# Performance work log

Hardware: AMD Instinct MI355X
Metric: run time of the kernel (lower is better)

## Reference

```python
import jax, jax.numpy as jnp
import numpy as np

# ---- static config (mirrors LSSTransform defaults) ----
B, N, CIN, CT = 4, 6, 512, 64
OGH, OGW, DS = 256, 704, 16
FH, FW = OGH // DS, OGW // DS            # 16, 44
DB0, DB1, DBS = 4.0, 45.0, 1.0
D = int((DB1 - DB0) / DBS)               # 41 depth bins
NXX, NYY, NZZ = 128, 128, 1              # BEV grid from x/y/z bounds
DXv = np.array([0.8, 0.8, 20.0], np.float32)            # dx
BXv = np.array([-51.2 + 0.4, -51.2 + 0.4, 0.0], np.float32)  # bx = lower + dx/2


def _frustum():
    # (D, fH, fW, 3) of (pixel_u, pixel_v, depth), as in create_frustum
    ds = np.broadcast_to(np.arange(DB0, DB1, DBS, dtype=np.float32)[:, None, None], (D, FH, FW))
    xs = np.broadcast_to(np.linspace(0, OGW - 1, FW, dtype=np.float32)[None, None, :], (D, FH, FW))
    ys = np.broadcast_to(np.linspace(0, OGH - 1, FH, dtype=np.float32)[None, :, None], (D, FH, FW))
    return jnp.asarray(np.stack([xs, ys, ds], axis=-1))

FRUSTUM = _frustum()


def setup_inputs() -> dict:
    key = jax.random.key(0)
    k0, k1, k2 = jax.random.split(key, 3)
    x = jax.random.normal(k0, (B, N, CIN, FH, FW), jnp.float32)
    # camera->ego rotation: ego = (z_cam, x_cam, y_cam), so depth maps to ego-x
    R = jnp.array([[0., 0., 1.], [1., 0., 0.], [0., 1., 0.]], jnp.float32)
    rots = jnp.broadcast_to(R, (B, N, 3, 3)) + 0.0
    trans = 0.5 * jax.random.normal(k1, (B, N, 3), jnp.float32)
    K = jnp.array([[500., 0., OGW / 2.], [0., 500., OGH / 2.], [0., 0., 1.]], jnp.float32)
    intrins = jnp.broadcast_to(K, (B, N, 3, 3)) + 0.0
    post_rots = jnp.broadcast_to(jnp.eye(3, dtype=jnp.float32), (B, N, 3, 3)) + 0.0
    post_trans = jnp.zeros((B, N, 3), jnp.float32)
    Wd = 0.02 * jax.random.normal(k2, (D + CT, CIN), jnp.float32)  # depthnet 1x1 conv weight
    bd = jnp.zeros((D + CT,), jnp.float32)
    return dict(x=x, rots=rots, trans=trans, intrins=intrins,
                post_rots=post_rots, post_trans=post_trans, Wd=Wd, bd=bd)


def _forward(x, rots, trans, intrins, post_rots, post_trans, Wd, bd):
    # depthnet: 1x1 conv == channel matmul
    feat = jnp.einsum('bnchw,oc->bnohw', x, Wd) + bd[None, None, :, None, None]
    depth = jax.nn.softmax(feat[:, :, :D], axis=2)          # (B,N,D,H,W)
    cvt = feat[:, :, D:D + CT]                              # (B,N,CT,H,W)
    vol = depth[:, :, None] * cvt[:, :, :, None]            # (B,N,CT,D,H,W)
    vol = jnp.transpose(vol, (0, 1, 3, 4, 5, 2))            # (B,N,D,H,W,CT)

    # get_geometry: undo image augs, unproject, cam->ego
    pts = FRUSTUM[None, None] - post_trans[:, :, None, None, None, :]
    pts = jnp.einsum('bnij,bndhwj->bndhwi', jnp.linalg.inv(post_rots), pts)
    pts = jnp.concatenate([pts[..., :2] * pts[..., 2:3], pts[..., 2:3]], axis=-1)
    comb = rots @ jnp.linalg.inv(intrins)
    pts = jnp.einsum('bnij,bndhwj->bndhwi', comb, pts) + trans[:, :, None, None, None, :]

    # voxel_pooling: truncating cast matches torch .long()
    g = ((pts - (jnp.asarray(BXv) - jnp.asarray(DXv) / 2.0)) / jnp.asarray(DXv)).astype(jnp.int32)
    gx, gy, gz = g[..., 0], g[..., 1], g[..., 2]
    kept = (gx >= 0) & (gx < NXX) & (gy >= 0) & (gy < NYY) & (gz >= 0) & (gz < NZZ)
    bix = jnp.arange(B, dtype=jnp.int32)[:, None, None, None, None]
    vox = ((bix * NZZ + gz) * NYY + gy) * NXX + gx          # flat voxel id per point
    TOT = B * NZZ * NYY * NXX
    seg = jnp.where(kept, vox, TOT).reshape(-1)             # invalid -> trash bucket
    feats = vol.reshape(-1, CT)                             # (Nprime, CT)
    sums = jax.ops.segment_sum(feats, seg, num_segments=TOT + 1)[:TOT]
    final = sums.reshape(B, NZZ, NYY, NXX, CT)
    # (B, C, nz, ny, nx) then cat over z into channels -> (B, nz*C, ny, nx)
    final = jnp.transpose(final, (0, 1, 4, 2, 3)).reshape(B, NZZ * CT, NYY, NXX)
    return final


def reference(x, rots, trans, intrins, post_rots, post_trans, Wd, bd):
    return _forward(x, rots, trans, intrins, post_rots, post_trans, Wd, bd)
```

## Files before the change

kernel.cpp:

```cpp
#include <hip/hip_runtime.h>
#include <hip/hip_bf16.h>
#include <math.h>

#define B_   4
#define N_   6
#define CIN  512
#define CT   64
#define Dd   41
#define FH   16
#define FW   44
#define NPIX 704
#define NO   105
#define DSTR 48
#define NXX  128
#define NYY  128
#define NZZ  1
#define TOT  (B_*NZZ*NYY*NXX)
#define NK   (TOT*8)
#define NPTS (B_*N_*Dd*NPIX)
#define NCHUNK ((NPTS+63)/64)

#define WSTRIDE 520

typedef __attribute__((ext_vector_type(8))) short short8;
typedef __attribute__((ext_vector_type(4))) float f32x4;


__device__ __forceinline__ unsigned short f2bf(float f) {
    unsigned u = __float_as_uint(f);
    u += 0x7FFFu + ((u >> 16) & 1u);
    return (unsigned short)(u >> 16);
}

__device__ __forceinline__ void inv3(const double* m, double* o) {
    double a=m[0],b=m[1],c=m[2],d=m[3],e=m[4],f=m[5],g=m[6],h=m[7],i=m[8];
    double A  =  (e*i - f*h);
    double Bc = -(d*i - f*g);
    double Cc =  (d*h - e*g);
    double det = a*A + b*Bc + c*Cc;
    double inv = 1.0/det;
    o[0]=A*inv;            o[1]=-(b*i - c*h)*inv;  o[2]= (b*f - c*e)*inv;
    o[3]=Bc*inv;           o[4]= (a*i - c*g)*inv;  o[5]=-(a*f - c*d)*inv;
    o[6]=Cc*inv;           o[7]=-(a*h - b*g)*inv;  o[8]= (a*e - b*d)*inv;
}

__device__ __forceinline__ void geom_lane(const double* s_tf, int b, int pix, int l,
                                          bool& kept, int& vox) {
    const int hh = pix / FW, ww = pix % FW;
    const double fx = (double)((float)(ww * (703.0/43.0)));
    const double fy = (double)((float)(hh * 17.0));
    const double px = fx - s_tf[21], py = fy - s_tf[22], mz = -s_tf[23];
    const double qx0 = s_tf[ 9]*px + s_tf[10]*py + s_tf[11]*mz, qx1 = s_tf[11];
    const double qy0 = s_tf[12]*px + s_tf[13]*py + s_tf[14]*mz, qy1 = s_tf[14];
    const double qz0 = s_tf[15]*px + s_tf[16]*py + s_tf[17]*mz, qz1 = s_tf[17];
    const double ux0 = s_tf[0]*qx0 + s_tf[1]*qy0 + s_tf[2], ux1 = s_tf[0]*qx1 + s_tf[1]*qy1;
    const double uy0 = s_tf[3]*qx0 + s_tf[4]*qy0 + s_tf[5], uy1 = s_tf[3]*qx1 + s_tf[4]*qy1;
    const double uz0 = s_tf[6]*qx0 + s_tf[7]*qy0 + s_tf[8], uz1 = s_tf[6]*qx1 + s_tf[7]*qy1;
    const double t0 = s_tf[18], t1 = s_tf[19], t2 = s_tf[20];

    const double DXD = (double)0.8f;
    const double LOX = (double)(-50.8f) - DXD*0.5;
    const double LOY = LOX;
    const double DZD = 20.0;
    const double LOZ = -10.0;

    kept = false; vox = 0;
    if (l < Dd) {
        double fz = 4.0 + (double)l;
        double qz = qz0 + qz1*fz;
        double sx = qz*(ux0 + ux1*fz) + t0;
        double sy = qz*(uy0 + uy1*fz) + t1;
        double sz = qz*(uz0 + uz1*fz) + t2;
        int gx = (int)((sx - LOX) / DXD);
        int gy = (int)((sy - LOY) / DXD);
        int gz = (int)((sz - LOZ) / DZD);
        kept = (gx>=0) & (gx<NXX) & (gy>=0) & (gy<NYY) & (gz>=0) & (gz<NZZ);
        vox  = (((b*NZZ + gz)*NYY + gy)*NXX + gx);
    }
}

__global__ __launch_bounds__(256) void prep_kernel(
    const float* __restrict__ rots, const float* __restrict__ trans,
    const float* __restrict__ intrins, const float* __restrict__ post_rots,
    const float* __restrict__ post_trans, const float* __restrict__ Wd,
    const float* __restrict__ x,
    double* __restrict__ tf, unsigned short* __restrict__ WdB,
    unsigned short* __restrict__ xB)
{
    const int t = threadIdx.x;
    if (blockIdx.x < 2112) {
        __shared__ float s_x[64*65];
        const int p    = blockIdx.x;
        const int bn   = p / 88;
        const int r    = p % 88;
        const int kg   = r / 11;
        const int tile = r % 11;
        const int pix0 = tile * 64;

        const float* src = x + ((size_t)bn*CIN + kg*64)*NPIX + pix0;
        #pragma unroll
        for (int i = 0; i < 16; i++) {
            int idx = i*256 + t;
            int k  = idx >> 6;
            int px = idx & 63;
            s_x[k*65 + px] = src[(size_t)k*NPIX + px];
        }
        __syncthreads();

        const int px  = t & 63;
        #pragma unroll
        for (int pass = 0; pass < 2; pass++) {
            int k8l = (t >> 6) + 4*pass;
            unsigned pk[4];
            #pragma unroll
            for (int i = 0; i < 4; i++) {
                float a = s_x[(k8l*8 + 2*i    )*65 + px];
                float c = s_x[(k8l*8 + 2*i + 1)*65 + px];
                pk[i] = (unsigned)f2bf(a) | ((unsigned)f2bf(c) << 16);
            }
            unsigned* dst = (unsigned*)&xB[(((size_t)(bn*64 + kg*8 + k8l))*NPIX + pix0 + px)*8];
            *(uint4*)dst = make_uint4(pk[0], pk[1], pk[2], pk[3]);
        }
    } else {
        int b2 = blockIdx.x - 2112;
        int idx = b2*256 + t;
        if (idx < 128*CIN) {
            int o = idx / CIN;
            WdB[idx] = (o < NO) ? f2bf(Wd[idx]) : (unsigned short)0;
        }
        if (b2 == 0 && t < B_*N_) {
            int bn = t;
            double k[9], pr[9], r[9], ik[9], ipr[9], c[9];
            for (int i=0;i<9;i++) { k[i]=intrins[bn*9+i]; pr[i]=post_rots[bn*9+i]; r[i]=rots[bn*9+i]; }
            inv3(k, ik);
            inv3(pr, ipr);
            for (int i=0;i<3;i++)
                for (int j=0;j<3;j++) {
                    double s = 0.0;
                    for (int kk=0;kk<3;kk++) s += r[i*3+kk]*ik[kk*3+j];
                    c[i*3+j] = s;
                }
            double* o = tf + bn*24;
            for (int i=0;i<9;i++) o[i]   = c[i];
            for (int i=0;i<9;i++) o[9+i] = ipr[i];
            for (int i=0;i<3;i++) o[18+i] = (double)trans[bn*3+i];
            for (int i=0;i<3;i++) o[21+i] = (double)post_trans[bn*3+i];
        }
    }
}

__global__ __launch_bounds__(256) void gemm_kernel(
    const unsigned short* __restrict__ xB, const unsigned short* __restrict__ WdB,
    const float* __restrict__ bd,
    float* __restrict__ featD, float* __restrict__ featB)
{
    __shared__ unsigned short s_wd[32*WSTRIDE];

    const int t    = threadIdx.x;
    const int l    = t & 63;
    const int wv   = t >> 6;
    const int col  = l & 15;
    const int quad = l >> 4;

    const int xcd = blockIdx.x & 7;
    const int q   = blockIdx.x >> 3;
    const int s   = q & 3;
    const int pg  = q >> 2;
    const int p   = pg*8 + xcd;
    const int bn   = p / 11;
    const int tile = p % 11;
    const int pix0 = tile * 64;

    {
        const int o  = t >> 3;
        const int c8 = t & 7;
        const unsigned short* srcw = WdB + (size_t)(s*32 + o)*CIN;
        #pragma unroll
        for (int i = 0; i < 8; i++) {
            int k = c8*8 + i*64;
            *(uint4*)&s_wd[o*WSTRIDE + k] = *(const uint4*)&srcw[k];
        }
    }
    __syncthreads();

    f32x4 acc[2];
    acc[0] = (f32x4){0.f,0.f,0.f,0.f};
    acc[1] = (f32x4){0.f,0.f,0.f,0.f};

    const int pix = pix0 + wv*16 + col;
    const unsigned short* xbase = xB + (((size_t)(bn*64) )*NPIX)*8;

    #pragma unroll
    for (int ks = 0; ks < 16; ks++) {
        const int k8 = ks*4 + quad;
        short8 bfr = *(const short8*)&xbase[((size_t)k8*NPIX + pix)*8];
        #pragma unroll
        for (int j = 0; j < 2; j++) {
            short8 afr = *(const short8*)&s_wd[(j*16 + col)*WSTRIDE + ks*32 + quad*8];
            acc[j] = __builtin_amdgcn_mfma_f32_16x16x32_bf16(afr, bfr, acc[j], 0, 0, 0);
        }
    }

    const size_t prow = (size_t)(bn*NPIX + pix);
    #pragma unroll
    for (int j = 0; j < 2; j++) {
        #pragma unroll
        for (int rr = 0; rr < 4; rr++) {
            int o = (2*s + j)*16 + quad*4 + rr;
            if (o < Dd) {
                featD[prow*DSTR + o] = acc[j][rr] + bd[o];
            } else if (o < NO) {
                featB[prow*CT + (o - Dd)] = acc[j][rr] + bd[o];
            }
        }
    }
}

__global__ __launch_bounds__(256) void geom_hist_kernel(
    const double* __restrict__ tf, int* __restrict__ hist8,
    int* __restrict__ rank_arr)
{
    __shared__ double s_tf[24];
    const int bid = (blockIdx.x & 7) * 528 + (blockIdx.x >> 3);
    const int t   = threadIdx.x;
    const int l   = t & 63;
    const int wv  = t >> 6;
    const int bn  = bid / 176;
    const int pix = (bid % 176)*4 + wv;
    const int b   = bn / N_;

    if (t < 24) s_tf[t] = tf[bn*24 + t];
    __syncthreads();

    bool kept; int vox;
    geom_lane(s_tf, b, pix, l, kept, vox);
    if (kept) {
        int key = vox*8 + (pix & 7);
        int rank = atomicAdd(&hist8[key], 1);
        rank_arr[(size_t)(bn*NPIX + pix)*Dd + l] = rank;
    }
}

__global__ __launch_bounds__(256) void scan1_kernel(const int* __restrict__ hist8,
                                                    int* __restrict__ offs8,
                                                    int* __restrict__ bsum) {
    __shared__ int s[256];
    const int t = threadIdx.x;
    const int i = blockIdx.x*256 + t;
    int val = hist8[i];
    s[t] = val;
    __syncthreads();
    #pragma unroll
    for (int off = 1; off < 256; off <<= 1) {
        int u = (t >= off) ? s[t-off] : 0;
        __syncthreads();
        s[t] += u;
        __syncthreads();
    }
    offs8[i] = s[t] - val;
    if (t == 255) bsum[blockIdx.x] = s[255];
}

__global__ __launch_bounds__(1024) void scan2_kernel(int* __restrict__ bsum,
                                                     int* __restrict__ np) {
    __shared__ int s[1024];
    const int t = threadIdx.x;
    int a = bsum[2*t], b = bsum[2*t+1];
    s[t] = a + b;
    __syncthreads();
    #pragma unroll
    for (int off = 1; off < 1024; off <<= 1) {
        int u = (t >= off) ? s[t-off] : 0;
        __syncthreads();
        s[t] += u;
        __syncthreads();
    }
    int excl = s[t] - (a + b);
    bsum[2*t]   = excl;
    bsum[2*t+1] = excl + a;
    if (t == 1023) np[0] = s[1023];
}

__global__ __launch_bounds__(256) void sm_scatter_kernel(
    const float* __restrict__ featD, const double* __restrict__ tf,
    const int* __restrict__ offs8, const int* __restrict__ bsum,
    const int* __restrict__ rank_arr, uint2* __restrict__ rec)
{
    __shared__ double s_tf[24];
    const int bid = (blockIdx.x & 7) * 528 + (blockIdx.x >> 3);
    const int t   = threadIdx.x;
    const int l   = t & 63;
    const int wv  = t >> 6;
    const int bn  = bid / 176;
    const int pix = (bid % 176)*4 + wv;
    const int b   = bn / N_;

    if (t < 24) s_tf[t] = tf[bn*24 + t];
    __syncthreads();

    const size_t prow = (size_t)(bn*NPIX + pix);

    float logit = (l < Dd) ? featD[prow*DSTR + l] : -3.0e38f;
    float mm = logit;
    #pragma unroll
    for (int off = 32; off > 0; off >>= 1) mm = fmaxf(mm, __shfl_xor(mm, off));
    float e = (l < Dd) ? expf(logit - mm) : 0.0f;
    float ssum = e;
    #pragma unroll
    for (int off = 32; off > 0; off >>= 1) ssum += __shfl_xor(ssum, off);
    const float wgt = e / ssum;

    bool kept; int vox;
    geom_lane(s_tf, b, pix, l, kept, vox);
    if (kept) {
        int key = vox*8 + (pix & 7);
        int pos = offs8[key] + bsum[key >> 8] + rank_arr[prow*Dd + l];
        unsigned pk = ((unsigned)vox << 15) | (unsigned)prow;
        rec[pos] = make_uint2(pk, __float_as_uint(wgt));
    }
}

__global__ __launch_bounds__(256) void gather_kernel(
    const uint2* __restrict__ rec, const int* __restrict__ np,
    const float* __restrict__ featB, float* __restrict__ scat)
{
    const int bid = (blockIdx.x & 7) * 339 + (blockIdx.x >> 3);
    const int t  = threadIdx.x;
    const int wv = t >> 6;
    const int l  = t & 63;
    const int chunk = bid * 4 + wv;
    const int base  = chunk * 64;
    const int Np = np[0];
    if (base >= Np) return;
    int cnt = Np - base; if (cnt > 64) cnt = 64;

    unsigned pk = 0; float w = 0.0f;
    if (l < cnt) { uint2 r = rec[base + l]; pk = r.x; w = __uint_as_float(r.y); }
    unsigned pkm = __shfl(pk, (l == 0) ? 0 : (l - 1));
    unsigned long long starts =
        __ballot((l > 0) && (l < cnt) && ((pk >> 15) != (pkm >> 15)));

    unsigned long long m = starts;
    int rs = 0;
    while (rs < cnt) {
        int re = m ? (__ffsll((unsigned long long)m) - 1) : cnt;
        if (m) m &= m - 1;
        float acc = 0.0f;
        for (int j = rs; j < re; j++) {
            unsigned pkj = __shfl(pk, j);
            float    wj  = __shfl(w, j);
            unsigned id  = pkj & 0x7FFFu;
            acc += wj * featB[(size_t)id * CT + l];
        }
        unsigned vrun = __shfl(pk, rs) >> 15;
        float* dst = scat + (size_t)vrun * CT + l;
        if (rs == 0 || re == cnt) {
            unsafeAtomicAdd(dst, acc);
        } else {
            *dst = acc;
        }
        rs = re;
    }
}

__global__ __launch_bounds__(256) void transpose_k(const float* __restrict__ scat,
                                                   float* __restrict__ out) {
    __shared__ float tile[64][65];
    int b  = blockIdx.x >> 8;
    int t0 = (blockIdx.x & 255) * 64;
    const float* src = scat + (size_t)b * (NYY*NXX) * CT;
    #pragma unroll
    for (int i=0;i<16;i++) {
        int idx = threadIdx.x + i*256;
        int p = idx >> 6, c = idx & 63;
        tile[p][c] = src[(size_t)(t0+p)*CT + c];
    }
    __syncthreads();
    float* dst = out + (size_t)b * CT * (NYY*NXX);
    #pragma unroll
    for (int i=0;i<16;i++) {
        int idx = threadIdx.x + i*256;
        int c = idx >> 6, p = idx & 63;
        dst[(size_t)c*(NYY*NXX) + t0 + p] = tile[p][c];
    }
}

extern "C" void kernel_launch(void* const* d_in, const int* in_sizes, int n_in,
                              void* d_out, int out_size, void* d_ws, size_t ws_size,
                              hipStream_t stream) {
    const float* x          = (const float*)d_in[0];
    const float* rots       = (const float*)d_in[1];
    const float* trans      = (const float*)d_in[2];
    const float* intrins    = (const float*)d_in[3];
    const float* post_rots  = (const float*)d_in[4];
    const float* post_trans = (const float*)d_in[5];
    const float* Wd         = (const float*)d_in[6];
    const float* bd         = (const float*)d_in[7];
    float* out = (float*)d_out;

    char* ws = (char*)d_ws;
    float*          featB  = (float*)ws;          ws += (size_t)B_*N_*NPIX*CT*4;
    float*          featD  = (float*)ws;          ws += (size_t)B_*N_*NPIX*DSTR*4;
    char*           Xreg   = ws;                  ws += (size_t)B_*N_*CIN*NPIX*2;
    int*            rank_a = (int*)ws;            ws += (size_t)NPTS*4;
    uint2*          rec    = (uint2*)ws;          ws += (size_t)NPTS*8;
    int*            hist8  = (int*)ws;            ws += (size_t)NK*4;
    int*            offs8  = (int*)ws;            ws += (size_t)NK*4;
    int*            bsum   = (int*)ws;            ws += 2048*4;
    int*            np     = (int*)ws;            ws += 256;
    double*         tf     = (double*)ws;         ws += (size_t)B_*N_*24*8;
    unsigned short* WdB    = (unsigned short*)ws; ws += (size_t)128*CIN*2;

    unsigned short* xB   = (unsigned short*)Xreg;
    float*          scat = (float*)Xreg;

    hipMemsetAsync(hist8, 0, (size_t)NK*4, stream);
    prep_kernel<<<2368, 256, 0, stream>>>(rots, trans, intrins, post_rots, post_trans,
                                          Wd, x, tf, WdB, xB);
    gemm_kernel<<<1056, 256, 0, stream>>>(xB, WdB, bd, featD, featB);
    geom_hist_kernel<<<B_*N_*176, 256, 0, stream>>>(tf, hist8, rank_a);
    hipMemsetAsync(scat, 0, (size_t)TOT*CT*4, stream);
    scan1_kernel<<<NK/256, 256, 0, stream>>>(hist8, offs8, bsum);
    scan2_kernel<<<1, 1024, 0, stream>>>(bsum, np);
    sm_scatter_kernel<<<B_*N_*176, 256, 0, stream>>>(featD, tf, offs8, bsum, rank_a, rec);
    gather_kernel<<<2712, 256, 0, stream>>>(rec, np, featB, scat);
    transpose_k<<<B_*(NYY*NXX/64), 256, 0, stream>>>(scat, out);
}
```

Baseline: 220.9 us.

## Fuse GEMM and geometry histogram launches, drop 8-way sub-bucketed histogram

Merges the depthnet GEMM and the geometry/histogram kernel into one launch whose blocks branch on their index, so the two independent stages can overlap on the GPU. The histogram is also reduced from eight sub-buckets per voxel (keyed by pixel) to one counter per voxel. This shrinks the memset, both scan passes and the offset lookups. In exchange, more atomics land on the same address, and the order in which records within a voxel are sorted changes.

```diff
diff --git a/kernel.cpp b/kernel.cpp
--- a/kernel.cpp
+++ b/kernel.cpp
@@ -16,11 +16,13 @@
 #define NYY  128
 #define NZZ  1
 #define TOT  (B_*NZZ*NYY*NXX)
-#define NK   (TOT*8)
 #define NPTS (B_*N_*Dd*NPIX)
 #define NCHUNK ((NPTS+63)/64)
 
 #define WSTRIDE 520
+
+#define GEMM_BLOCKS 1056
+#define GEOM_BLOCKS 4224
 
 typedef __attribute__((ext_vector_type(8))) short short8;
 typedef __attribute__((ext_vector_type(4))) float f32x4;
@@ -149,105 +151,100 @@
     }
 }
 
-__global__ __launch_bounds__(256) void gemm_kernel(
+__global__ __launch_bounds__(256) void gemm_geom_kernel(
     const unsigned short* __restrict__ xB, const unsigned short* __restrict__ WdB,
-    const float* __restrict__ bd,
-    float* __restrict__ featD, float* __restrict__ featB)
+    const float* __restrict__ bd, const double* __restrict__ tf,
+    float* __restrict__ featD, float* __restrict__ featB,
+    int* __restrict__ hist, int* __restrict__ rank_arr)
 {
     __shared__ unsigned short s_wd[32*WSTRIDE];
+    __shared__ double s_tf[24];
 
     const int t    = threadIdx.x;
     const int l    = t & 63;
     const int wv   = t >> 6;
-    const int col  = l & 15;
-    const int quad = l >> 4;
-
-    const int xcd = blockIdx.x & 7;
-    const int q   = blockIdx.x >> 3;
-    const int s   = q & 3;
-    const int pg  = q >> 2;
-    const int p   = pg*8 + xcd;
-    const int bn   = p / 11;
-    const int tile = p % 11;
-    const int pix0 = tile * 64;
-
-    {
-        const int o  = t >> 3;
-        const int c8 = t & 7;
-        const unsigned short* srcw = WdB + (size_t)(s*32 + o)*CIN;
+
+    if (blockIdx.x < GEMM_BLOCKS) {
+        const int col  = l & 15;
+        const int quad = l >> 4;
+        const int xcd = blockIdx.x & 7;
+        const int q   = blockIdx.x >> 3;
+        const int s   = q & 3;
+        const int pg  = q >> 2;
+        const int p   = pg*8 + xcd;
+        const int bn   = p / 11;
+        const int tile = p % 11;
+        const int pix0 = tile * 64;
+
+        {
+            const int o  = t >> 3;
+            const int c8 = t & 7;
+            const unsigned short* srcw = WdB + (size_t)(s*32 + o)*CIN;
+            #pragma unroll
+            for (int i = 0; i < 8; i++) {
+                int k = c8*8 + i*64;
+                *(uint4*)&s_wd[o*WSTRIDE + k] = *(const uint4*)&srcw[k];
+            }
+        }
+        __syncthreads();
+
+        f32x4 acc[2];
+        acc[0] = (f32x4){0.f,0.f,0.f,0.f};
+        acc[1] = (f32x4){0.f,0.f,0.f,0.f};
+
+        const int pix = pix0 + wv*16 + col;
+        const unsigned short* xbase = xB + (((size_t)(bn*64))*NPIX)*8;
+
         #pragma unroll
-        for (int i = 0; i < 8; i++) {
-            int k = c8*8 + i*64;
-            *(uint4*)&s_wd[o*WSTRIDE + k] = *(const uint4*)&srcw[k];
-        }
-    }
-    __syncthreads();
-
-    f32x4 acc[2];
-    acc[0] = (f32x4){0.f,0.f,0.f,0.f};
-    acc[1] = (f32x4){0.f,0.f,0.f,0.f};
-
-    const int pix = pix0 + wv*16 + col;
-    const unsigned short* xbase = xB + (((size_t)(bn*64) )*NPIX)*8;
-
-    #pragma unroll
-    for (int ks = 0; ks < 16; ks++) {
-        const int k8 = ks*4 + quad;
-        short8 bfr = *(const short8*)&xbase[((size_t)k8*NPIX + pix)*8];
+        for (int ks = 0; ks < 16; ks++) {
+            const int k8 = ks*4 + quad;
+            short8 bfr = *(const short8*)&xbase[((size_t)k8*NPIX + pix)*8];
+            #pragma unroll
+            for (int j = 0; j < 2; j++) {
+                short8 afr = *(const short8*)&s_wd[(j*16 + col)*WSTRIDE + ks*32 + quad*8];
+                acc[j] = __builtin_amdgcn_mfma_f32_16x16x32_bf16(afr, bfr, acc[j], 0, 0, 0);
+            }
+        }
+
+        const size_t prow = (size_t)(bn*NPIX + pix);
         #pragma unroll
         for (int j = 0; j < 2; j++) {
-            short8 afr = *(const short8*)&s_wd[(j*16 + col)*WSTRIDE + ks*32 + quad*8];
-            acc[j] = __builtin_amdgcn_mfma_f32_16x16x32_bf16(afr, bfr, acc[j], 0, 0, 0);
-        }
-    }
-
-    const size_t prow = (size_t)(bn*NPIX + pix);
-    #pragma unroll
-    for (int j = 0; j < 2; j++) {
-        #pragma unroll
-        for (int rr = 0; rr < 4; rr++) {
-            int o = (2*s + j)*16 + quad*4 + rr;
-            if (o < Dd) {
-                featD[prow*DSTR + o] = acc[j][rr] + bd[o];
-            } else if (o < NO) {
-                featB[prow*CT + (o - Dd)] = acc[j][rr] + bd[o];
+            #pragma unroll
+            for (int rr = 0; rr < 4; rr++) {
+                int o = (2*s + j)*16 + quad*4 + rr;
+                if (o < Dd) {
+                    featD[prow*DSTR + o] = acc[j][rr] + bd[o];
+                } else if (o < NO) {
+                    featB[prow*CT + (o - Dd)] = acc[j][rr] + bd[o];
+                }
             }
         }
-    }
-}
-
-__global__ __launch_bounds__(256) void geom_hist_kernel(
-    const double* __restrict__ tf, int* __restrict__ hist8,
-    int* __restrict__ rank_arr)
-{
-    __shared__ double s_tf[24];
-    const int bid = (blockIdx.x & 7) * 528 + (blockIdx.x >> 3);
-    const int t   = threadIdx.x;
-    const int l   = t & 63;
-    const int wv  = t >> 6;
-    const int bn  = bid / 176;
-    const int pix = (bid % 176)*4 + wv;
-    const int b   = bn / N_;
-
-    if (t < 24) s_tf[t] = tf[bn*24 + t];
-    __syncthreads();
-
-    bool kept; int vox;
-    geom_lane(s_tf, b, pix, l, kept, vox);
-    if (kept) {
-        int key = vox*8 + (pix & 7);
-        int rank = atomicAdd(&hist8[key], 1);
-        rank_arr[(size_t)(bn*NPIX + pix)*Dd + l] = rank;
-    }
-}
-
-__global__ __launch_bounds__(256) void scan1_kernel(const int* __restrict__ hist8,
-                                                    int* __restrict__ offs8,
+    } else {
+        const int bid2 = blockIdx.x - GEMM_BLOCKS;
+        const int bid  = (bid2 & 7) * 528 + (bid2 >> 3);
+        const int bn  = bid / 176;
+        const int pix = (bid % 176)*4 + wv;
+        const int b   = bn / N_;
+
+        if (t < 24) s_tf[t] = tf[bn*24 + t];
+        __syncthreads();
+
+        bool kept; int vox;
+        geom_lane(s_tf, b, pix, l, kept, vox);
+        if (kept) {
+            int rank = atomicAdd(&hist[vox], 1);
+            rank_arr[(size_t)(bn*NPIX + pix)*Dd + l] = rank;
+        }
+    }
+}
+
+__global__ __launch_bounds__(256) void scan1_kernel(const int* __restrict__ hist,
+                                                    int* __restrict__ offs,
                                                     int* __restrict__ bsum) {
     __shared__ int s[256];
     const int t = threadIdx.x;
     const int i = blockIdx.x*256 + t;
-    int val = hist8[i];
+    int val = hist[i];
     s[t] = val;
     __syncthreads();
     #pragma unroll
@@ -257,33 +254,31 @@
         s[t] += u;
         __syncthreads();
     }
-    offs8[i] = s[t] - val;
+    offs[i] = s[t] - val;
     if (t == 255) bsum[blockIdx.x] = s[255];
 }
 
-__global__ __launch_bounds__(1024) void scan2_kernel(int* __restrict__ bsum,
-                                                     int* __restrict__ np) {
-    __shared__ int s[1024];
+__global__ __launch_bounds__(256) void scan2_kernel(int* __restrict__ bsum,
+                                                    int* __restrict__ np) {
+    __shared__ int s[256];
     const int t = threadIdx.x;
-    int a = bsum[2*t], b = bsum[2*t+1];
-    s[t] = a + b;
+    int v = bsum[t];
+    s[t] = v;
     __syncthreads();
     #pragma unroll
-    for (int off = 1; off < 1024; off <<= 1) {
+    for (int off = 1; off < 256; off <<= 1) {
         int u = (t >= off) ? s[t-off] : 0;
         __syncthreads();
         s[t] += u;
         __syncthreads();
     }
-    int excl = s[t] - (a + b);
-    bsum[2*t]   = excl;
-    bsum[2*t+1] = excl + a;
-    if (t == 1023) np[0] = s[1023];
+    bsum[t] = s[t] - v;
+    if (t == 255) np[0] = s[255];
 }
 
 __global__ __launch_bounds__(256) void sm_scatter_kernel(
     const float* __restrict__ featD, const double* __restrict__ tf,
-    const int* __restrict__ offs8, const int* __restrict__ bsum,
+    const int* __restrict__ offs, const int* __restrict__ bsum,
     const int* __restrict__ rank_arr, uint2* __restrict__ rec)
 {
     __shared__ double s_tf[24];
@@ -313,8 +308,7 @@
     bool kept; int vox;
     geom_lane(s_tf, b, pix, l, kept, vox);
     if (kept) {
-        int key = vox*8 + (pix & 7);
-        int pos = offs8[key] + bsum[key >> 8] + rank_arr[prow*Dd + l];
+        int pos = offs[vox] + bsum[vox >> 8] + rank_arr[prow*Dd + l];
         unsigned pk = ((unsigned)vox << 15) | (unsigned)prow;
         rec[pos] = make_uint2(pk, __float_as_uint(wgt));
     }
@@ -404,9 +398,9 @@
     char*           Xreg   = ws;                  ws += (size_t)B_*N_*CIN*NPIX*2;
     int*            rank_a = (int*)ws;            ws += (size_t)NPTS*4;
     uint2*          rec    = (uint2*)ws;          ws += (size_t)NPTS*8;
-    int*            hist8  = (int*)ws;            ws += (size_t)NK*4;
-    int*            offs8  = (int*)ws;            ws += (size_t)NK*4;
-    int*            bsum   = (int*)ws;            ws += 2048*4;
+    int*            hist   = (int*)ws;            ws += (size_t)TOT*4;
+    int*            offs   = (int*)ws;            ws += (size_t)TOT*4;
+    int*            bsum   = (int*)ws;            ws += 256*4;
     int*            np     = (int*)ws;            ws += 256;
     double*         tf     = (double*)ws;         ws += (size_t)B_*N_*24*8;
     unsigned short* WdB    = (unsigned short*)ws; ws += (size_t)128*CIN*2;
@@ -414,15 +408,15 @@
     unsigned short* xB   = (unsigned short*)Xreg;
     float*          scat = (float*)Xreg;
 
-    hipMemsetAsync(hist8, 0, (size_t)NK*4, stream);
+    hipMemsetAsync(hist, 0, (size_t)TOT*4, stream);
     prep_kernel<<<2368, 256, 0, stream>>>(rots, trans, intrins, post_rots, post_trans,
                                           Wd, x, tf, WdB, xB);
-    gemm_kernel<<<1056, 256, 0, stream>>>(xB, WdB, bd, featD, featB);
-    geom_hist_kernel<<<B_*N_*176, 256, 0, stream>>>(tf, hist8, rank_a);
+    gemm_geom_kernel<<<GEMM_BLOCKS + GEOM_BLOCKS, 256, 0, stream>>>(
+        xB, WdB, bd, tf, featD, featB, hist, rank_a);
     hipMemsetAsync(scat, 0, (size_t)TOT*CT*4, stream);
-    scan1_kernel<<<NK/256, 256, 0, stream>>>(hist8, offs8, bsum);
-    scan2_kernel<<<1, 1024, 0, stream>>>(bsum, np);
-    sm_scatter_kernel<<<B_*N_*176, 256, 0, stream>>>(featD, tf, offs8, bsum, rank_a, rec);
+    scan1_kernel<<<TOT/256, 256, 0, stream>>>(hist, offs, bsum);
+    scan2_kernel<<<1, 256, 0, stream>>>(bsum, np);
+    sm_scatter_kernel<<<B_*N_*176, 256, 0, stream>>>(featD, tf, offs, bsum, rank_a, rec);
     gather_kernel<<<2712, 256, 0, stream>>>(rec, np, featB, scat);
     transpose_k<<<B_*(NYY*NXX/64), 256, 0, stream>>>(scat, out);
 }
```

Result: faster. 208.9 us (-5.4%).
